# Optimization experiments

Hardware: AMD Instinct MI355X
Metric: run time of the kernel (lower is better)

Reference implementation:

```python
import jax, jax.numpy as jnp
import numpy as np

COSINE_SIM_SCALE = 8.0  # default scale in flash-cosine-sim-attention
LN_EPS = 1e-5
HEADS = 8

def _l2norm(t, eps=1e-12):
    return t * jax.lax.rsqrt(jnp.sum(t * t, axis=-1, keepdims=True) + eps)

def setup_inputs() -> dict:
    key = jax.random.key(0)
    k1, k2, k3 = jax.random.split(key, 3)
    b, n, dim = 2, 2048, 1024
    inner = 512  # heads * dim_head
    return {
        "x": jax.random.normal(k1, (b, n, dim), dtype=jnp.float32),
        "ln_w": jnp.ones((dim,), dtype=jnp.float32),
        "ln_b": jnp.zeros((dim,), dtype=jnp.float32),
        "w_qkv": jax.random.normal(k2, (dim, 3 * inner), dtype=jnp.float32) * 0.02,
        "w_out": jax.random.normal(k3, (inner, dim), dtype=jnp.float32) * 0.02,
    }

def reference(x, ln_w, ln_b, w_qkv, w_out):
    b, n, dim = x.shape
    h = HEADS
    # LayerNorm
    mu = jnp.mean(x, axis=-1, keepdims=True)
    var = jnp.mean(jnp.square(x - mu), axis=-1, keepdims=True)
    xn = (x - mu) * jax.lax.rsqrt(var + LN_EPS) * ln_w + ln_b
    # QKV projection, split into heads: b n (h d) -> b h n d
    qkv = xn @ w_qkv
    q, k, v = jnp.split(qkv, 3, axis=-1)
    def to_heads(t):
        return t.reshape(b, n, h, -1).transpose(0, 2, 1, 3)
    q, k, v = map(to_heads, (q, k, v))
    # cosine-sim attention: l2-normalize q, k then scaled dot product
    q = _l2norm(q)
    k = _l2norm(k)
    sim = jnp.einsum('bhid,bhjd->bhij', q, k) * COSINE_SIM_SCALE
    causal_mask = jnp.tril(jnp.ones((n, n), dtype=bool))
    sim = jnp.where(causal_mask, sim, jnp.finfo(sim.dtype).min)
    attn = jax.nn.softmax(sim, axis=-1)
    o = jnp.einsum('bhij,bhjd->bhid', attn, v)
    # b h n d -> b n (h d)
    o = o.transpose(0, 2, 1, 3).reshape(b, n, -1)
    return o @ w_out
```

## Files before the change

### kernel.cpp

```cpp
#include <hip/hip_runtime.h>
#include <hip/hip_bf16.h>

typedef __attribute__((ext_vector_type(8))) __bf16 bf16x8;
typedef __attribute__((ext_vector_type(4))) __bf16 bf16x4;
typedef __attribute__((ext_vector_type(4))) float f32x4;

#define B_     2
#define N_     2048
#define DIM_   1024
#define INNER_ 512
#define H_     8
#define DH_    64
#define ROWS_  (B_ * N_)
#define QKVN_  (3 * INNER_)
#define SEGROWS_ 5120
#define QSCALE_ 11.5415603f
#define MAXL2_  11.5415603f

static __device__ __forceinline__ f32x4 mfma16(bf16x8 a, bf16x8 b, f32x4 c) {
    return __builtin_amdgcn_mfma_f32_16x16x32_bf16(a, b, c, 0, 0, 0);
}

static __device__ __forceinline__ void gld_lds16(const void* g, void* l) {
    __builtin_amdgcn_global_load_lds((const __attribute__((address_space(1))) void*)g,
                                     (__attribute__((address_space(3))) void*)l, 16, 0, 0);
}

__global__ __launch_bounds__(256) void prep_kernel(const float* __restrict__ x,
                                                   const float* __restrict__ lnw,
                                                   const float* __restrict__ lnb,
                                                   const float* __restrict__ wqkv,
                                                   const float* __restrict__ wout,
                                                   __bf16* __restrict__ xn,
                                                   __bf16* __restrict__ wqkvT,
                                                   __bf16* __restrict__ woutT) {
    int bid = blockIdx.x;
    int tid = threadIdx.x;
    if (bid < ROWS_) {
        int row = bid;
        const float* xr = x + (size_t)row * DIM_;
        f32x4 xv = *reinterpret_cast<const f32x4*>(xr + tid * 4);
        float s  = xv.x + xv.y + xv.z + xv.w;
        float sq = xv.x * xv.x + xv.y * xv.y + xv.z * xv.z + xv.w * xv.w;
#pragma unroll
        for (int m = 1; m < 64; m <<= 1) {
            s  += __shfl_xor(s, m);
            sq += __shfl_xor(sq, m);
        }
        __shared__ float red[2][4];
        int wid = tid >> 6, lane = tid & 63;
        if (lane == 0) { red[0][wid] = s; red[1][wid] = sq; }
        __syncthreads();
        s  = red[0][0] + red[0][1] + red[0][2] + red[0][3];
        sq = red[1][0] + red[1][1] + red[1][2] + red[1][3];
        float mu   = s * (1.0f / DIM_);
        float var  = sq * (1.0f / DIM_) - mu * mu;
        float rstd = rsqrtf(var + 1e-5f);
        f32x4 wv = *reinterpret_cast<const f32x4*>(lnw + tid * 4);
        f32x4 bv = *reinterpret_cast<const f32x4*>(lnb + tid * 4);
        bf16x4 o;
#pragma unroll
        for (int j = 0; j < 4; ++j) o[j] = (__bf16)((xv[j] - mu) * rstd * wv[j] + bv[j]);
        *reinterpret_cast<bf16x4*>(xn + (size_t)row * DIM_ + tid * 4) = o;
        return;
    }
    __shared__ float t[64][65];
    bid -= ROWS_;
    const float* in; __bf16* out; int K, N, bx, by;
    if (bid < 384) { in = wqkv; out = wqkvT; K = DIM_;   N = QKVN_; bx = bid % 24; by = bid / 24; }
    else { bid -= 384; in = wout; out = woutT; K = INNER_; N = DIM_;  bx = bid % 16; by = bid / 16; }
    int n0 = bx * 64, k0 = by * 64;
    int w = tid >> 6, lane = tid & 63;
#pragma unroll
    for (int i = 0; i < 16; ++i) {
        int k = 16 * w + i;
        t[k][lane] = in[(size_t)(k0 + k) * N + n0 + lane];
    }
    __syncthreads();
#pragma unroll
    for (int i = 0; i < 16; ++i) {
        int n = 16 * w + i;
        out[(size_t)(n0 + n) * K + k0 + lane] = (__bf16)t[lane][n];
    }
}

__global__ __launch_bounds__(256) void gemm_qkv(const __bf16* __restrict__ A,
                                                const __bf16* __restrict__ Bt,
                                                __bf16* __restrict__ Qh,
                                                __bf16* __restrict__ Kh,
                                                __bf16* __restrict__ Vrow) {
    const int K = DIM_;
    __shared__ __bf16 As[2][128 * 64];
    __shared__ __bf16 Bs[2][64 * 64];
    int id = blockIdx.x;
    int nid = (id & 7) * 96 + (id >> 3);
    int bx = nid % 24, by = nid / 24;
    int tid = threadIdx.x;
    int w = tid >> 6, lane = tid & 63;
    int lr = lane & 15, lg = lane >> 4;
    int m0 = by * 128, n0 = bx * 64;
    int sr = tid >> 3, sc8 = tid & 7;
    const __bf16* Ab = A  + (size_t)m0 * K;
    const __bf16* Bb = Bt + (size_t)n0 * K;
    f32x4 acc[2][4];
#pragma unroll
    for (int mi = 0; mi < 2; ++mi)
#pragma unroll
        for (int ci = 0; ci < 4; ++ci) acc[mi][ci] = f32x4{0.f, 0.f, 0.f, 0.f};

    auto stage = [&](int buf, int k0) {
#pragma unroll
        for (int i = 0; i < 4; ++i) {
            int r = sr + i * 32;
            int cs = sc8 ^ (r & 7);
            gld_lds16(Ab + (size_t)r * K + k0 + 8 * cs, &As[buf][r * 64 + sc8 * 8]);
        }
#pragma unroll
        for (int i = 0; i < 2; ++i) {
            int r = sr + i * 32;
            int cs = sc8 ^ (r & 7);
            gld_lds16(Bb + (size_t)r * K + k0 + 8 * cs, &Bs[buf][r * 64 + sc8 * 8]);
        }
    };

    stage(0, 0);
    __syncthreads();
    int cur = 0;
    for (int k0 = 0; k0 < K; k0 += 64) {
        if (k0 + 64 < K) stage(cur ^ 1, k0 + 64);
        bf16x8 af[2][2], bfr[2][4];
#pragma unroll
        for (int kk = 0; kk < 2; ++kk) {
#pragma unroll
            for (int mi = 0; mi < 2; ++mi) {
                int r = w * 32 + 16 * mi + lr;
                af[kk][mi] = *reinterpret_cast<const bf16x8*>(
                    &As[cur][r * 64 + 8 * ((kk * 4 + lg) ^ (r & 7))]);
            }
#pragma unroll
            for (int ci = 0; ci < 4; ++ci) {
                int r = 16 * ci + lr;
                bfr[kk][ci] = *reinterpret_cast<const bf16x8*>(
                    &Bs[cur][r * 64 + 8 * ((kk * 4 + lg) ^ (r & 7))]);
            }
        }
#pragma unroll
        for (int kk = 0; kk < 2; ++kk)
#pragma unroll
            for (int mi = 0; mi < 2; ++mi)
#pragma unroll
                for (int ci = 0; ci < 4; ++ci)
                    acc[mi][ci] = mfma16(af[kk][mi], bfr[kk][ci], acc[mi][ci]);
        __syncthreads();
        cur ^= 1;
    }
    int u = bx;
    bool isV = (u >= 16);
    float smul = (u < 8) ? QSCALE_ : 1.0f;
    __bf16* base;
    if (u < 8)       base = Qh   + (size_t)u * N_ * DH_;
    else if (u < 16) base = Kh   + (size_t)(u - 8) * N_ * DH_;
    else             base = Vrow + (size_t)(u - 16) * N_ * DH_;
#pragma unroll
    for (int mi = 0; mi < 2; ++mi)
#pragma unroll
        for (int r = 0; r < 4; ++r) {
            int grow = m0 + w * 32 + 16 * mi + 4 * lg + r;
            int b = grow >> 11, n = grow & 2047;
            float sc2 = 1.0f;
            if (!isV) {
                float t = 0.f;
#pragma unroll
                for (int ci = 0; ci < 4; ++ci) t += acc[mi][ci][r] * acc[mi][ci][r];
#pragma unroll
                for (int m = 1; m < 16; m <<= 1) t += __shfl_xor(t, m);
                sc2 = rsqrtf(t + 1e-12f) * smul;
            }
            __bf16* dst = base + ((size_t)b * H_ * N_ + n) * DH_;
#pragma unroll
            for (int ci = 0; ci < 4; ++ci)
                dst[16 * ci + lr] = (__bf16)(acc[mi][ci][r] * sc2);
        }
}

__global__ __launch_bounds__(256) void vtrans(const __bf16* __restrict__ Vrow,
                                              __bf16* __restrict__ Vt) {
    __shared__ __bf16 t[64][66];
    int bh = blockIdx.y, n0 = blockIdx.x * 64;
    int w = threadIdx.x >> 6, lane = threadIdx.x & 63;
#pragma unroll
    for (int i = 0; i < 16; ++i) {
        int nl = 16 * w + i;
        t[nl][lane] = Vrow[((size_t)bh * N_ + n0 + nl) * DH_ + lane];
    }
    __syncthreads();
#pragma unroll
    for (int i = 0; i < 16; ++i) {
        int d = 16 * w + i;
        Vt[(size_t)bh * DH_ * N_ + (size_t)d * N_ + n0 + lane] = t[lane][d];
    }
}

__global__ __launch_bounds__(256) void attn_kernel(const __bf16* __restrict__ Qh,
                                                   const __bf16* __restrict__ Kh,
                                                   const __bf16* __restrict__ Vt,
                                                   float* __restrict__ Opart,
                                                   float* __restrict__ lpart) {
    __shared__ __bf16 Ks[2][64 * 64];
    __shared__ __bf16 Vs[64 * 64];
    __shared__ __bf16 pl[4][16 * 64];
    int xcd = blockIdx.x & 7;
    int q   = blockIdx.x >> 3;
    int bh  = xcd * 2 + (q & 1);
    int sid = q >> 1;
    int s, qt;
    if (sid < 32)      { s = 0; qt = 31 - sid; }
    else if (sid < 56) { s = 1; qt = 31 - (sid - 32); }
    else if (sid < 72) { s = 2; qt = 31 - (sid - 56); }
    else               { s = 3; qt = 31 - (sid - 72); }
    int jt0 = 8 * s;
    int jt1 = min(8 * s + 7, qt);
    int tid = threadIdx.x;
    int w = tid >> 6, lane = tid & 63;
    int lr = lane & 15, lg = lane >> 4;
    int qrow = qt * 64 + 16 * w;
    const __bf16* Qp = Qh + (size_t)bh * N_ * DH_;
    const __bf16* Kp = Kh + (size_t)bh * N_ * DH_;
    const __bf16* Vp = Vt + (size_t)bh * DH_ * N_;
    bf16x8 qf0 = *reinterpret_cast<const bf16x8*>(Qp + (size_t)(qrow + lr) * DH_ + 8 * lg);
    bf16x8 qf1 = *reinterpret_cast<const bf16x8*>(Qp + (size_t)(qrow + lr) * DH_ + 32 + 8 * lg);
    bf16x8 ones;
#pragma unroll
    for (int j = 0; j < 8; ++j) ones[j] = (__bf16)1.0f;
    f32x4 oacc[4];
    f32x4 oacc4 = f32x4{0.f, 0.f, 0.f, 0.f};
#pragma unroll
    for (int c = 0; c < 4; ++c) oacc[c] = f32x4{0.f, 0.f, 0.f, 0.f};
    int srow = tid >> 3, sc = tid & 7;

    auto stageK = [&](int buf, int jb) {
#pragma unroll
        for (int qq = 0; qq < 2; ++qq) {
            int row = qq * 32 + srow;
            int cs = sc ^ (row & 7);
            gld_lds16(Kp + (size_t)(jb + row) * DH_ + 8 * cs,
                      &Ks[buf][(size_t)row * 64 + sc * 8]);
        }
    };
    auto stageV = [&](int jb) {
#pragma unroll
        for (int qq = 0; qq < 2; ++qq) {
            int row = qq * 32 + srow;
            int cs = sc ^ (row & 7);
            gld_lds16(Vp + (size_t)row * N_ + jb + 8 * cs,
                      &Vs[(size_t)row * 64 + sc * 8]);
        }
    };

    stageK(0, jt0 * 64);
    stageV(jt0 * 64);
    __syncthreads();
    int cur = 0;
    for (int jt = jt0; jt <= jt1; ++jt) {
        int jb = jt * 64;
        if (jt < jt1) stageK(cur ^ 1, jb + 64);
        const __bf16* ks = &Ks[cur][0];
        f32x4 sm[4];
#pragma unroll
        for (int ch = 0; ch < 4; ++ch) {
            int row = 16 * ch + lr;
            bf16x8 k0 = *reinterpret_cast<const bf16x8*>(&ks[row * 64 + 8 * (lg ^ (row & 7))]);
            bf16x8 k1 = *reinterpret_cast<const bf16x8*>(&ks[row * 64 + 8 * ((4 + lg) ^ (row & 7))]);
            f32x4 t = f32x4{0.f, 0.f, 0.f, 0.f};
            t = mfma16(qf0, k0, t);
            t = mfma16(qf1, k1, t);
            sm[ch] = t;
        }
        f32x4 p[4];
        bool diag = (jt == qt);
#pragma unroll
        for (int ch = 0; ch < 4; ++ch)
#pragma unroll
            for (int r = 0; r < 4; ++r) {
                float pv = exp2f(sm[ch][r] - MAXL2_);
                if (diag) {
                    int qi = qrow + 4 * lg + r;
                    int j  = jb + 16 * ch + lr;
                    if (j > qi) pv = 0.f;
                }
                p[ch][r] = pv;
            }
        __bf16* plw = &pl[w][0];
#pragma unroll
        for (int ch = 0; ch < 4; ++ch)
#pragma unroll
            for (int r = 0; r < 4; ++r) {
                int row = 4 * lg + r, col = 16 * ch + lr;
                plw[row * 64 + (((col >> 3) ^ (row & 7)) << 3) + (col & 7)] = (__bf16)p[ch][r];
            }
        bf16x8 pf0 = *reinterpret_cast<const bf16x8*>(&plw[lr * 64 + ((lg ^ (lr & 7)) << 3)]);
        bf16x8 pf1 = *reinterpret_cast<const bf16x8*>(&plw[lr * 64 + (((4 + lg) ^ (lr & 7)) << 3)]);
        __syncthreads();
#pragma unroll
        for (int dc = 0; dc < 4; ++dc) {
            int row = 16 * dc + lr;
            bf16x8 v0 = *reinterpret_cast<const bf16x8*>(&Vs[row * 64 + 8 * (lg ^ (row & 7))]);
            bf16x8 v1 = *reinterpret_cast<const bf16x8*>(&Vs[row * 64 + 8 * ((4 + lg) ^ (row & 7))]);
            oacc[dc] = mfma16(pf0, v0, oacc[dc]);
            oacc[dc] = mfma16(pf1, v1, oacc[dc]);
        }
        oacc4 = mfma16(pf0, ones, oacc4);
        oacc4 = mfma16(pf1, ones, oacc4);
        __syncthreads();
        if (jt < jt1) stageV(jb + 64);
        cur ^= 1;
    }
    int soff = 2048 * s - 256 * s * (s - 1);
#pragma unroll
    for (int r = 0; r < 4; ++r) {
        int n = qrow + 4 * lg + r;
        size_t ridx = (size_t)bh * SEGROWS_ + soff + (n - 512 * s);
#pragma unroll
        for (int dc = 0; dc < 4; ++dc)
            Opart[ridx * 64 + 16 * dc + lr] = oacc[dc][r];
        if (lr == 0) lpart[ridx] = oacc4[r];
    }
}

__global__ __launch_bounds__(256) void combine_kernel(const float* __restrict__ Opart,
                                                      const float* __restrict__ lpart,
                                                      __bf16* __restrict__ Obp) {
    int gid = blockIdx.x * 4 + (threadIdx.x >> 6);
    int lane = threadIdx.x & 63;
    int bh = gid >> 11, n = gid & 2047;
    int smax = n >> 9;
    float acc = 0.f, lsum = 0.f;
#pragma unroll
    for (int s = 0; s < 4; ++s)
        if (s <= smax) {
            int soff = 2048 * s - 256 * s * (s - 1);
            size_t ridx = (size_t)bh * SEGROWS_ + soff + (n - 512 * s);
            acc  += Opart[ridx * 64 + lane];
            lsum += lpart[ridx];
        }
    int b = bh >> 3, h = bh & 7;
    Obp[((size_t)(b * N_ + n)) * INNER_ + h * DH_ + lane] = (__bf16)(acc / lsum);
}

__global__ __launch_bounds__(256) void gemm_out(const __bf16* __restrict__ A,
                                                const __bf16* __restrict__ Bt,
                                                float* __restrict__ C) {
    const int K = INNER_, N = DIM_;
    __shared__ __bf16 As[2][64 * 64];
    __shared__ __bf16 Bs[2][64 * 64];
    int id = blockIdx.x;
    int nid = (id & 7) * 128 + (id >> 3);
    int bx = nid % 16, by = nid / 16;
    int tid = threadIdx.x;
    int w = tid >> 6, lane = tid & 63;
    int lr = lane & 15, lg = lane >> 4;
    int m0 = by * 64, n0 = bx * 64;
    int sr = tid >> 3, sc8 = tid & 7;
    const __bf16* Ab = A  + (size_t)m0 * K;
    const __bf16* Bb = Bt + (size_t)n0 * K;
    f32x4 acc[4];
#pragma unroll
    for (int ci = 0; ci < 4; ++ci) acc[ci] = f32x4{0.f, 0.f, 0.f, 0.f};

    auto stage = [&](int buf, int k0) {
#pragma unroll
        for (int i = 0; i < 2; ++i) {
            int r = sr + i * 32;
            int cs = sc8 ^ (r & 7);
            gld_lds16(Ab + (size_t)r * K + k0 + 8 * cs, &As[buf][r * 64 + sc8 * 8]);
            gld_lds16(Bb + (size_t)r * K + k0 + 8 * cs, &Bs[buf][r * 64 + sc8 * 8]);
        }
    };

    stage(0, 0);
    __syncthreads();
    int cur = 0;
    for (int k0 = 0; k0 < K; k0 += 64) {
        if (k0 + 64 < K) stage(cur ^ 1, k0 + 64);
        bf16x8 af[2], bfr[2][4];
#pragma unroll
        for (int kk = 0; kk < 2; ++kk) {
            int r = w * 16 + lr;
            af[kk] = *reinterpret_cast<const bf16x8*>(
                &As[cur][r * 64 + 8 * ((kk * 4 + lg) ^ (r & 7))]);
#pragma unroll
            for (int ci = 0; ci < 4; ++ci) {
                int rb = 16 * ci + lr;
                bfr[kk][ci] = *reinterpret_cast<const bf16x8*>(
                    &Bs[cur][rb * 64 + 8 * ((kk * 4 + lg) ^ (rb & 7))]);
            }
        }
#pragma unroll
        for (int kk = 0; kk < 2; ++kk)
#pragma unroll
            for (int ci = 0; ci < 4; ++ci)
                acc[ci] = mfma16(af[kk], bfr[kk][ci], acc[ci]);
        __syncthreads();
        cur ^= 1;
    }
#pragma unroll
    for (int ci = 0; ci < 4; ++ci)
#pragma unroll
        for (int r = 0; r < 4; ++r)
            C[(size_t)(m0 + w * 16 + 4 * lg + r) * N + n0 + 16 * ci + lr] = acc[ci][r];
}

extern "C" void kernel_launch(void* const* d_in, const int* in_sizes, int n_in,
                              void* d_out, int out_size, void* d_ws, size_t ws_size,
                              hipStream_t stream) {
    const float* x    = (const float*)d_in[0];
    const float* lnw  = (const float*)d_in[1];
    const float* lnb  = (const float*)d_in[2];
    const float* wqkv = (const float*)d_in[3];
    const float* wout = (const float*)d_in[4];
    float* out = (float*)d_out;

    char* ws = (char*)d_ws;
    size_t off = 0;
    auto alloc = [&](size_t bytes) -> char* {
        char* p = ws + off;
        off += (bytes + 255) & ~(size_t)255;
        return p;
    };
    __bf16* xn    = (__bf16*)alloc((size_t)ROWS_ * DIM_ * 2);
    __bf16* wqkvT = (__bf16*)alloc((size_t)QKVN_ * DIM_ * 2);
    __bf16* woutT = (__bf16*)alloc((size_t)DIM_ * INNER_ * 2);
    __bf16* Qhp   = (__bf16*)alloc((size_t)B_ * H_ * N_ * DH_ * 2);
    __bf16* Khp   = (__bf16*)alloc((size_t)B_ * H_ * N_ * DH_ * 2);
    __bf16* Vrow  = (__bf16*)alloc((size_t)B_ * H_ * N_ * DH_ * 2);
    __bf16* Vtp   = (__bf16*)alloc((size_t)B_ * H_ * DH_ * N_ * 2);
    __bf16* Obp   = (__bf16*)alloc((size_t)ROWS_ * INNER_ * 2);
    float*  Opart = (float*)alloc((size_t)B_ * H_ * SEGROWS_ * DH_ * 4);
    float*  lbuf  = (float*)alloc((size_t)B_ * H_ * SEGROWS_ * 4);
    if (off > ws_size) return;

    prep_kernel<<<ROWS_ + 512, 256, 0, stream>>>(x, lnw, lnb, wqkv, wout, xn, wqkvT, woutT);
    gemm_qkv<<<768, 256, 0, stream>>>(xn, wqkvT, Qhp, Khp, Vrow);
    vtrans<<<dim3(N_ / 64, B_ * H_), 256, 0, stream>>>(Vrow, Vtp);
    attn_kernel<<<1280, 256, 0, stream>>>(Qhp, Khp, Vtp, Opart, lbuf);
    combine_kernel<<<(ROWS_ * H_) / 4, 256, 0, stream>>>(Opart, lbuf, Obp);
    gemm_out<<<1024, 256, 0, stream>>>(Obp, woutT, out);
}
```

Baseline: 153.8 us.

## Load V fragments directly from global to registers and store partial outputs as bf16

The attention kernel no longer stages V tiles in shared memory. Each wave loads its V MFMA fragments straight from global memory into registers at the start of each key tile, which removes the V LDS buffer and one block-wide barrier per iteration. Partial outputs are also written in bf16 rather than fp32, halving the traffic between the attention and combine kernels. The trade-offs are redundant global loads of V across the four waves, a possible stall waiting on those loads, and lower precision in the partial sums.

```diff
diff --git a/kernel.cpp b/kernel.cpp
--- a/kernel.cpp
+++ b/kernel.cpp
@@ -204,10 +204,9 @@
 __global__ __launch_bounds__(256) void attn_kernel(const __bf16* __restrict__ Qh,
                                                    const __bf16* __restrict__ Kh,
                                                    const __bf16* __restrict__ Vt,
-                                                   float* __restrict__ Opart,
+                                                   __bf16* __restrict__ Opart,
                                                    float* __restrict__ lpart) {
     __shared__ __bf16 Ks[2][64 * 64];
-    __shared__ __bf16 Vs[64 * 64];
     __shared__ __bf16 pl[4][16 * 64];
     int xcd = blockIdx.x & 7;
     int q   = blockIdx.x >> 3;
@@ -247,23 +246,20 @@
                       &Ks[buf][(size_t)row * 64 + sc * 8]);
         }
     };
-    auto stageV = [&](int jb) {
-#pragma unroll
-        for (int qq = 0; qq < 2; ++qq) {
-            int row = qq * 32 + srow;
-            int cs = sc ^ (row & 7);
-            gld_lds16(Vp + (size_t)row * N_ + jb + 8 * cs,
-                      &Vs[(size_t)row * 64 + sc * 8]);
-        }
-    };
 
     stageK(0, jt0 * 64);
-    stageV(jt0 * 64);
     __syncthreads();
     int cur = 0;
     for (int jt = jt0; jt <= jt1; ++jt) {
         int jb = jt * 64;
         if (jt < jt1) stageK(cur ^ 1, jb + 64);
+        bf16x8 vv0[4], vv1[4];
+#pragma unroll
+        for (int dc = 0; dc < 4; ++dc) {
+            int row = 16 * dc + lr;
+            vv0[dc] = *reinterpret_cast<const bf16x8*>(Vp + (size_t)row * N_ + jb + 8 * lg);
+            vv1[dc] = *reinterpret_cast<const bf16x8*>(Vp + (size_t)row * N_ + jb + 32 + 8 * lg);
+        }
         const __bf16* ks = &Ks[cur][0];
         f32x4 sm[4];
 #pragma unroll
@@ -300,19 +296,14 @@
             }
         bf16x8 pf0 = *reinterpret_cast<const bf16x8*>(&plw[lr * 64 + ((lg ^ (lr & 7)) << 3)]);
         bf16x8 pf1 = *reinterpret_cast<const bf16x8*>(&plw[lr * 64 + (((4 + lg) ^ (lr & 7)) << 3)]);
-        __syncthreads();
 #pragma unroll
         for (int dc = 0; dc < 4; ++dc) {
-            int row = 16 * dc + lr;
-            bf16x8 v0 = *reinterpret_cast<const bf16x8*>(&Vs[row * 64 + 8 * (lg ^ (row & 7))]);
-            bf16x8 v1 = *reinterpret_cast<const bf16x8*>(&Vs[row * 64 + 8 * ((4 + lg) ^ (row & 7))]);
-            oacc[dc] = mfma16(pf0, v0, oacc[dc]);
-            oacc[dc] = mfma16(pf1, v1, oacc[dc]);
+            oacc[dc] = mfma16(pf0, vv0[dc], oacc[dc]);
+            oacc[dc] = mfma16(pf1, vv1[dc], oacc[dc]);
         }
         oacc4 = mfma16(pf0, ones, oacc4);
         oacc4 = mfma16(pf1, ones, oacc4);
         __syncthreads();
-        if (jt < jt1) stageV(jb + 64);
         cur ^= 1;
     }
     int soff = 2048 * s - 256 * s * (s - 1);
@@ -322,12 +313,12 @@
         size_t ridx = (size_t)bh * SEGROWS_ + soff + (n - 512 * s);
 #pragma unroll
         for (int dc = 0; dc < 4; ++dc)
-            Opart[ridx * 64 + 16 * dc + lr] = oacc[dc][r];
+            Opart[ridx * 64 + 16 * dc + lr] = (__bf16)oacc[dc][r];
         if (lr == 0) lpart[ridx] = oacc4[r];
     }
 }
 
-__global__ __launch_bounds__(256) void combine_kernel(const float* __restrict__ Opart,
+__global__ __launch_bounds__(256) void combine_kernel(const __bf16* __restrict__ Opart,
                                                       const float* __restrict__ lpart,
                                                       __bf16* __restrict__ Obp) {
     int gid = blockIdx.x * 4 + (threadIdx.x >> 6);
@@ -340,7 +331,7 @@
         if (s <= smax) {
             int soff = 2048 * s - 256 * s * (s - 1);
             size_t ridx = (size_t)bh * SEGROWS_ + soff + (n - 512 * s);
-            acc  += Opart[ridx * 64 + lane];
+            acc  += (float)Opart[ridx * 64 + lane];
             lsum += lpart[ridx];
         }
     int b = bh >> 3, h = bh & 7;
@@ -435,7 +426,7 @@
     __bf16* Vrow  = (__bf16*)alloc((size_t)B_ * H_ * N_ * DH_ * 2);
     __bf16* Vtp   = (__bf16*)alloc((size_t)B_ * H_ * DH_ * N_ * 2);
     __bf16* Obp   = (__bf16*)alloc((size_t)ROWS_ * INNER_ * 2);
-    float*  Opart = (float*)alloc((size_t)B_ * H_ * SEGROWS_ * DH_ * 4);
+    __bf16* Opart = (__bf16*)alloc((size_t)B_ * H_ * SEGROWS_ * DH_ * 2);
     float*  lbuf  = (float*)alloc((size_t)B_ * H_ * SEGROWS_ * 4);
     if (off > ws_size) return;
 
```

After: 167.9 us. +9.2%, slower.
